# Kernel optimization log

Measured on AMD Instinct MI355X. Metric: run time of the kernel, lower is better.

Reference implementation:

```python
import jax, jax.numpy as jnp
import numpy as np

B, DIM, H, W = 8, 64, 64, 64
N_EMBED = 512
NNZ = 4          # num_nonzero OMP iterations
REG = 1e-7       # tiny Tikhonov term for the batched normal-equation solves


def batch_omp(X, D, S):
    """Batch OMP: for each signal pick S atoms greedily and solve LS on support.
    X: [N, d] signals, D: [d, K] dictionary with unit-norm atoms.
    Returns dense sparse code [N, K] with <= S nonzeros per row.
    Mathematically equivalent to the incremental-Cholesky Batch_OMP: at each
    step we solve G_II gamma = alpha0_I on the current support I.
    """
    N, K = X.shape[0], D.shape[1]
    G = D.T @ D                 # [K, K] Gram matrix (precomputed once)
    alpha0 = X @ D              # [N, K] initial correlations D^T x
    alpha = alpha0
    idx_cols = []
    gamma = None
    idx = None
    for k in range(S):          # static small loop over sparsity level
        j = jnp.argmax(jnp.abs(alpha), axis=1)                # [N] greedy atom
        idx_cols.append(j)
        idx = jnp.stack(idx_cols, axis=1)                     # [N, k+1]
        G_sub = G[idx[:, :, None], idx[:, None, :]]           # [N, k+1, k+1]
        rhs = jnp.take_along_axis(alpha0, idx, axis=1)        # [N, k+1]
        reg = REG * jnp.eye(k + 1, dtype=G.dtype)
        gamma = jnp.linalg.solve(G_sub + reg, rhs[..., None])[..., 0]  # [N, k+1]
        # residual correlations: alpha = alpha0 - G[:, I] gamma  (G symmetric)
        alpha = alpha0 - jnp.einsum('nak,na->nk', G[idx], gamma)
    code = jnp.zeros((N, K), X.dtype).at[jnp.arange(N)[:, None], idx].set(gamma)
    return code


def setup_inputs() -> dict:
    key = jax.random.key(0)
    kx, kd = jax.random.split(key)
    x = jax.random.normal(kx, (B, DIM, H, W), dtype=jnp.float32)
    dictionary = jax.random.normal(kd, (DIM, N_EMBED), dtype=jnp.float32)
    return {"x": x, "dictionary": dictionary}


def reference(x, dictionary):
    perm = jnp.transpose(x, (0, 2, 3, 1))            # [B, H, W, C]
    flat = perm.reshape(-1, DIM)                     # [N, C], N = B*H*W
    # normalize_dict=True: atoms normalized to unit L2 norm (in-place in torch)
    Dn = dictionary / jnp.linalg.norm(dictionary, axis=0, keepdims=True)
    code = batch_omp(flat, Dn, NNZ)                  # [N, K] (torch keeps [K, N])
    quant = (code @ Dn.T).reshape(perm.shape)        # reconstruction
    diff_enc = jnp.mean((quant - perm) ** 2)
    diff_dict = diff_enc                             # backward_dict=False branch
    # straight-through: perm + (quant - perm).detach() == quant in value
    out = jnp.transpose(quant, (0, 3, 1, 2))         # [B, C, H, W]
    ids = jnp.transpose(code.reshape(B, H, W, N_EMBED), (0, 3, 1, 2))  # [B, K, H, W]
    norm_0 = jnp.sum(code != 0, axis=1).astype(jnp.float32)  # L0 per signal, [N]
    num_steps = jnp.float32(NNZ)
    mean_D = jnp.mean(jnp.abs(Dn))
    mean_Z = jnp.mean(jnp.abs(code))
    norm_Z = jnp.mean(norm_0)
    topk_num = max(1, int(norm_0.shape[0] * 0.01))   # static: 327
    top_percentile = jnp.min(jax.lax.top_k(norm_0, topk_num)[0])
    num_zeros = jnp.sum(norm_0 == 0).astype(jnp.float32)
    return (out, diff_enc, diff_dict, ids, num_steps, mean_D, mean_Z,
            norm_Z, top_percentile, num_zeros)
```

## Files before the change

### kernel.cpp

```cpp
#include <hip/hip_runtime.h>
#include <cstdint>
#include <cstddef>

#define BQ 8
#define CDIM 64
#define HQ 64
#define WQ 64
#define KDIM 512
#define N_SIG 32768
#define S_NNZ 4

#define DIFF_ENC_OFF 2097152
#define DIFF_DICT_OFF 2097153
#define IDS_OFF 2097154
#define NUM_STEPS_OFF 18874370
#define MEAN_D_OFF 18874371
#define MEAN_Z_OFF 18874372
#define NORM_Z_OFF 18874373
#define TOP_PCT_OFF 18874374
#define NUM_ZEROS_OFF 18874375

#define WS_PD 16
#define WS_DNT 24
#define WS_G 32792
#define WS_WG 294936
#define WS_WI 426008

typedef float v2f __attribute__((ext_vector_type(2)));

__global__ __launch_bounds__(256) void k_ga(const float* __restrict__ X,
                                            const float* __restrict__ D,
                                            float* __restrict__ A0,
                                            float* __restrict__ G,
                                            float* __restrict__ DnT,
                                            float* __restrict__ pd,
                                            float* __restrict__ W) {
  __shared__ float Xs[64 * 64];
  __shared__ float Dns[64 * 64];
  __shared__ float partA[4][64];
  __shared__ float partB[4][64];
  __shared__ float invA[64];
  __shared__ float invB[64];
  int tid = threadIdx.x;
  int w = tid & 63, cq = tid >> 6;
  int ty = tid >> 4, tx = tid & 15;
  if (blockIdx.x == 0 && tid < 16) ((unsigned int*)W)[tid] = 0u;

  if (blockIdx.x < 64) {
    int ti = (int)blockIdx.x >> 3, tj = (int)blockIdx.x & 7;
#pragma unroll
    for (int p = 0; p < 16; ++p) {
      int c = p * 4 + cq;
      Xs[c * 64 + w] = D[(size_t)c * KDIM + ti * 64 + w];
      Dns[c * 64 + w] = D[(size_t)c * KDIM + tj * 64 + w];
    }
    __syncthreads();
    float ssA = 0.f, ssB = 0.f;
#pragma unroll
    for (int cc = 0; cc < 16; ++cc) {
      int c = cq * 16 + cc;
      float a = Xs[c * 64 + w];
      ssA = fmaf(a, a, ssA);
      float bv = Dns[c * 64 + w];
      ssB = fmaf(bv, bv, ssB);
    }
    partA[cq][w] = ssA;
    partB[cq][w] = ssB;
    __syncthreads();
    if (tid < 64) {
      invA[tid] = 1.0f / sqrtf(partA[0][tid] + partA[1][tid] + partA[2][tid] + partA[3][tid]);
      invB[tid] = 1.0f / sqrtf(partB[0][tid] + partB[1][tid] + partB[2][tid] + partB[3][tid]);
    }
    __syncthreads();
    if (ti == tj) {
      int kl = tid >> 2, cp = (tid & 3) * 16;
      float ia = invA[kl];
      float sabs = 0.f;
#pragma unroll
      for (int i = 0; i < 16; ++i) {
        int c = cp + i;
        float v = Xs[c * 64 + kl] * ia;
        DnT[(size_t)(ti * 64 + kl) * CDIM + c] = v;
        sabs += fabsf(v);
      }
#pragma unroll
      for (int off = 32; off >= 1; off >>= 1) sabs += __shfl_xor(sabs, off);
      __syncthreads();
      if ((tid & 63) == 0) partA[0][tid >> 6] = sabs;
      __syncthreads();
      if (tid == 0) pd[ti] = partA[0][0] + partA[0][1] + partA[0][2] + partA[0][3];
    }
    v2f acc[4][2] = {};
    for (int c = 0; c < 64; ++c) {
      float4 avv = *(const float4*)&Xs[c * 64 + ty * 4];
      float av[4] = {avv.x, avv.y, avv.z, avv.w};
      float4 bv = *(const float4*)&Dns[c * 64 + tx * 4];
      v2f b0 = {bv.x, bv.y}, b1 = {bv.z, bv.w};
#pragma unroll
      for (int i = 0; i < 4; ++i) {
        v2f a2 = {av[i], av[i]};
        acc[i][0] = __builtin_elementwise_fma(a2, b0, acc[i][0]);
        acc[i][1] = __builtin_elementwise_fma(a2, b1, acc[i][1]);
      }
    }
    float sn[4] = {invB[tx * 4], invB[tx * 4 + 1], invB[tx * 4 + 2], invB[tx * 4 + 3]};
#pragma unroll
    for (int i = 0; i < 4; ++i) {
      float im = invA[ty * 4 + i];
      float4 st = make_float4(acc[i][0].x * im * sn[0], acc[i][0].y * im * sn[1],
                              acc[i][1].x * im * sn[2], acc[i][1].y * im * sn[3]);
      *(float4*)&G[(size_t)(ti * 64 + ty * 4 + i) * KDIM + tj * 64 + tx * 4] = st;
    }
  } else {
    int bb = (int)blockIdx.x - 64;
    int mt = bb >> 3, nt = bb & 7;
    int b = mt >> 6, h = mt & 63;
#pragma unroll
    for (int p = 0; p < 16; ++p) {
      int c = p * 4 + cq;
      Xs[c * 64 + w] = X[(((size_t)b * CDIM + c) * HQ + h) * WQ + w];
      Dns[c * 64 + w] = D[(size_t)c * KDIM + nt * 64 + w];
    }
    __syncthreads();
    float ssB = 0.f;
#pragma unroll
    for (int cc = 0; cc < 16; ++cc) {
      int c = cq * 16 + cc;
      float bv = Dns[c * 64 + w];
      ssB = fmaf(bv, bv, ssB);
    }
    partB[cq][w] = ssB;
    __syncthreads();
    if (tid < 64)
      invB[tid] = 1.0f / sqrtf(partB[0][tid] + partB[1][tid] + partB[2][tid] + partB[3][tid]);
    __syncthreads();
    v2f acc[4][2] = {};
    for (int c = 0; c < 64; ++c) {
      float4 avv = *(const float4*)&Xs[c * 64 + ty * 4];
      float av[4] = {avv.x, avv.y, avv.z, avv.w};
      float4 bv = *(const float4*)&Dns[c * 64 + tx * 4];
      v2f b0 = {bv.x, bv.y}, b1 = {bv.z, bv.w};
#pragma unroll
      for (int i = 0; i < 4; ++i) {
        v2f a2 = {av[i], av[i]};
        acc[i][0] = __builtin_elementwise_fma(a2, b0, acc[i][0]);
        acc[i][1] = __builtin_elementwise_fma(a2, b1, acc[i][1]);
      }
    }
    float sn[4] = {invB[tx * 4], invB[tx * 4 + 1], invB[tx * 4 + 2], invB[tx * 4 + 3]};
    size_t n0 = (size_t)mt * 64;
#pragma unroll
    for (int i = 0; i < 4; ++i) {
      float4 st = make_float4(acc[i][0].x * sn[0], acc[i][0].y * sn[1],
                              acc[i][1].x * sn[2], acc[i][1].y * sn[3]);
      *(float4*)&A0[(n0 + ty * 4 + i) * KDIM + nt * 64 + tx * 4] = st;
    }
  }
}

__device__ __forceinline__ float wave_absmax_u(float m) {
#define DPP_MAX(ctrl)                                                              \
  {                                                                                \
    int t_ = __builtin_amdgcn_update_dpp(0, __float_as_int(m), (ctrl), 0xf, 0xf,   \
                                         true);                                    \
    m = fmaxf(m, __int_as_float(t_));                                              \
  }
  DPP_MAX(0x111) DPP_MAX(0x112) DPP_MAX(0x114) DPP_MAX(0x118)
  DPP_MAX(0x142) DPP_MAX(0x143)
#undef DPP_MAX
  return __int_as_float(__builtin_amdgcn_readlane(__float_as_int(m), 63));
}

template <int SZ>
__device__ __forceinline__ void solve_sz(const float (&gs)[4][4], const float (&rhs)[4],
                                         float (&gamma)[4]) {
  float M[SZ][SZ];
  float y[SZ];
  float idg[SZ];
#pragma unroll
  for (int a = 0; a < SZ; ++a) {
    y[a] = rhs[a];
#pragma unroll
    for (int b = 0; b < SZ; ++b) M[a][b] = gs[a][b] + (a == b ? 1e-7f : 0.0f);
  }
#pragma unroll
  for (int p = 0; p < SZ; ++p) {
    float ip = __builtin_amdgcn_rcpf(M[p][p]);
    idg[p] = ip;
#pragma unroll
    for (int r = p + 1; r < SZ; ++r) {
      float f = M[r][p] * ip;
#pragma unroll
      for (int c = p + 1; c < SZ; ++c) M[r][c] = fmaf(-f, M[p][c], M[r][c]);
      y[r] = fmaf(-f, y[p], y[r]);
    }
  }
#pragma unroll
  for (int r = SZ - 1; r >= 0; --r) {
    float t = y[r];
#pragma unroll
    for (int c = r + 1; c < SZ; ++c) t = fmaf(-M[r][c], gamma[c], t);
    gamma[r] = t * idg[r];
  }
}

template <int K>
__device__ __forceinline__ void omp_step(int lane, int n, const float* __restrict__ G,
                                         const float* __restrict__ A0,
                                         float (&a0)[8], float (&al)[8], float (&Grow)[3][8],
                                         float (&gs)[4][4], float (&rhs)[4], int (&idx)[4],
                                         float (&gamma)[4]) {
  float mx0 = fabsf(al[0]);
#pragma unroll
  for (int m = 1; m < 8; ++m) mx0 = fmaxf(mx0, fabsf(al[m]));
  float mx = wave_absmax_u(mx0);
  int sk = 1 << 30;
#pragma unroll
  for (int m = 0; m < 8; ++m) {
    unsigned long long bm = __ballot(fabsf(al[m]) == mx);
    if (bm) {
      int kk = (int)__builtin_ctzll(bm) * 8 + m;
      sk = kk < sk ? kk : sk;
    }
  }
  idx[K] = sk;

  const float* grow_base = G + (size_t)sk * KDIM;
  if constexpr (K < 3) {
    const float4* gp = (const float4*)(grow_base + lane * 8);
    float4 r0 = gp[0], r1 = gp[1];
    Grow[K][0] = r0.x; Grow[K][1] = r0.y; Grow[K][2] = r0.z; Grow[K][3] = r0.w;
    Grow[K][4] = r1.x; Grow[K][5] = r1.y; Grow[K][6] = r1.z; Grow[K][7] = r1.w;
  }

#pragma unroll
  for (int b = 0; b < K; ++b) {
    float v = grow_base[idx[b]];
    gs[K][b] = v;
    gs[b][K] = v;
  }
  gs[K][K] = grow_base[sk];
  rhs[K] = A0[(size_t)n * KDIM + sk];

  solve_sz<K + 1>(gs, rhs, gamma);

  if constexpr (K < 3) {
#pragma unroll
    for (int m = 0; m < 8; ++m) {
      float acc = a0[m];
#pragma unroll
      for (int a = 0; a <= K; ++a) acc = fmaf(-gamma[a], Grow[a][m], acc);
      al[m] = acc;
    }
  }
}

__global__ __launch_bounds__(256) void k_omp(const float* __restrict__ A0,
                                             const float* __restrict__ G,
                                             float4* __restrict__ wg, int4* __restrict__ wi) {
  int tid = threadIdx.x;
  int lane = tid & 63;
  int wv = __builtin_amdgcn_readfirstlane(tid >> 6);
  int n = blockIdx.x * 4 + wv;
  const float4* ap = (const float4*)(A0 + (size_t)n * KDIM + lane * 8);
  float4 v0 = ap[0], v1 = ap[1];
  float a0[8] = {v0.x, v0.y, v0.z, v0.w, v1.x, v1.y, v1.z, v1.w};
  float al[8];
#pragma unroll
  for (int m = 0; m < 8; ++m) al[m] = a0[m];
  float Grow[3][8];
  float gs[4][4];
  float rhs[4];
  int idx[4];
  float gamma[4];
  omp_step<0>(lane, n, G, A0, a0, al, Grow, gs, rhs, idx, gamma);
  omp_step<1>(lane, n, G, A0, a0, al, Grow, gs, rhs, idx, gamma);
  omp_step<2>(lane, n, G, A0, a0, al, Grow, gs, rhs, idx, gamma);
  omp_step<3>(lane, n, G, A0, a0, al, Grow, gs, rhs, idx, gamma);
  bool k0 = (idx[0] != idx[1]) && (idx[0] != idx[2]) && (idx[0] != idx[3]);
  bool k1 = (idx[1] != idx[2]) && (idx[1] != idx[3]);
  bool k2 = (idx[2] != idx[3]);
  if (lane == 0) {
    wg[n] = make_float4(k0 ? gamma[0] : 0.f, k1 ? gamma[1] : 0.f,
                        k2 ? gamma[2] : 0.f, gamma[3]);
    wi[n] = make_int4(idx[0], idx[1], idx[2], idx[3]);
  }
}

__global__ __launch_bounds__(256) void k_ei(const float* __restrict__ X,
                                            const float* __restrict__ DnT,
                                            const float4* __restrict__ wg,
                                            const int4* __restrict__ wi,
                                            float* __restrict__ out,
                                            double* __restrict__ accs,
                                            int* __restrict__ hist) {
  __shared__ __align__(16) int sIdx[64][4];
  __shared__ __align__(16) float sKg[64][4];
  __shared__ float q[64 * 65];
  __shared__ float red[4];
  int tid = threadIdx.x;

  if (blockIdx.x < 512) {
    int bh = blockIdx.x;
    int b = bh >> 6, h = bh & 63;
    if (tid < 64) {
      int w = tid;
      int n = bh * 64 + w;
      int4 iv = wi[n];
      float4 gv = wg[n];
      sIdx[w][0] = iv.x; sIdx[w][1] = iv.y; sIdx[w][2] = iv.z; sIdx[w][3] = iv.w;
      sKg[w][0] = gv.x; sKg[w][1] = gv.y; sKg[w][2] = gv.z; sKg[w][3] = gv.w;
      int nz = (int)(gv.x != 0.f) + (int)(gv.y != 0.f) +
               (int)(gv.z != 0.f) + (int)(gv.w != 0.f);
      float s = fabsf(gv.x) + fabsf(gv.y) + fabsf(gv.z) + fabsf(gv.w);
#pragma unroll
      for (int off = 32; off >= 1; off >>= 1) s += __shfl_xor(s, off);
#pragma unroll
      for (int v = 0; v < 5; ++v) {
        unsigned long long m = __ballot(nz == v);
        if (tid == 0) {
          int c = (int)__popcll(m);
          if (c) atomicAdd(&hist[v], c);
        }
      }
      if (tid == 0) atomicAdd(&accs[0], (double)s);
    }
    __syncthreads();

    int w2 = tid & 63, p = tid >> 6, c0 = p * 16;
    float acc[16] = {};
#pragma unroll
    for (int s = 0; s < 4; ++s) {
      int ks = sIdx[w2][s];
      float g = sKg[w2][s];
      const float4* dp = (const float4*)(DnT + (size_t)ks * CDIM + c0);
#pragma unroll
      for (int i4 = 0; i4 < 4; ++i4) {
        float4 d = dp[i4];
        acc[i4 * 4 + 0] = fmaf(g, d.x, acc[i4 * 4 + 0]);
        acc[i4 * 4 + 1] = fmaf(g, d.y, acc[i4 * 4 + 1]);
        acc[i4 * 4 + 2] = fmaf(g, d.z, acc[i4 * 4 + 2]);
        acc[i4 * 4 + 3] = fmaf(g, d.w, acc[i4 * 4 + 3]);
      }
    }
#pragma unroll
    for (int i = 0; i < 16; ++i) q[(c0 + i) * 65 + w2] = acc[i];
    __syncthreads();

    float sumsq = 0.f;
#pragma unroll
    for (int pass = 0; pass < 16; ++pass) {
      int c = pass * 4 + p;
      float qv = q[c * 65 + w2];
      size_t off = (((size_t)b * CDIM + c) * HQ + h) * WQ + w2;
      float xv = X[off];
      float d = qv - xv;
      sumsq = fmaf(d, d, sumsq);
      out[off] = qv;
    }

#pragma unroll
    for (int off = 32; off >= 1; off >>= 1) sumsq += __shfl_xor(sumsq, off);
    if ((tid & 63) == 0) red[tid >> 6] = sumsq;
    __syncthreads();
    if (tid == 0) atomicAdd(&accs[1], (double)(red[0] + red[1] + red[2] + red[3]));
  } else {
    int bid = blockIdx.x - 512;
    int bh = bid >> 2, kq = bid & 3;
    int b = bh >> 6, h = bh & 63;
    if (tid < 64) {
      int n = bh * 64 + tid;
      *(int4*)&sIdx[tid][0] = wi[n];
      *(float4*)&sKg[tid][0] = wg[n];
    }
    __syncthreads();
    int w4 = (tid & 15) * 4, kl = tid >> 4;
    int4 I0 = *(const int4*)&sIdx[w4][0];
    int4 I1 = *(const int4*)&sIdx[w4 + 1][0];
    int4 I2 = *(const int4*)&sIdx[w4 + 2][0];
    int4 I3 = *(const int4*)&sIdx[w4 + 3][0];
    float4 G0 = *(const float4*)&sKg[w4][0];
    float4 G1 = *(const float4*)&sKg[w4 + 1][0];
    float4 G2 = *(const float4*)&sKg[w4 + 2][0];
    float4 G3 = *(const float4*)&sKg[w4 + 3][0];
    float* ids = out + IDS_OFF;
    size_t base = (((size_t)b * KDIM + kq * 128 + kl) * HQ + h) * WQ + w4;
#pragma unroll
    for (int pass = 0; pass < 8; ++pass) {
      int k = kq * 128 + pass * 16 + kl;
      float4 v;
      v.x = (k == I0.w) ? G0.w : (k == I0.z) ? G0.z : (k == I0.y) ? G0.y : (k == I0.x) ? G0.x : 0.f;
      v.y = (k == I1.w) ? G1.w : (k == I1.z) ? G1.z : (k == I1.y) ? G1.y : (k == I1.x) ? G1.x : 0.f;
      v.z = (k == I2.w) ? G2.w : (k == I2.z) ? G2.z : (k == I2.y) ? G2.y : (k == I2.x) ? G2.x : 0.f;
      v.w = (k == I3.w) ? G3.w : (k == I3.z) ? G3.z : (k == I3.y) ? G3.y : (k == I3.x) ? G3.x : 0.f;
      *(float4*)&ids[base + (size_t)pass * 16 * 4096] = v;
    }
  }
}

__global__ __launch_bounds__(64) void k_final(const double* __restrict__ accs,
                                              const int* __restrict__ hist,
                                              const float* __restrict__ pd,
                                              float* __restrict__ out) {
  if (threadIdx.x == 0) {
    float sumAbsD = 0.f;
#pragma unroll
    for (int i = 0; i < 8; ++i) sumAbsD += pd[i];
    double sumAbsZ = accs[0], sumSq = accs[1];
    float diff = (float)(sumSq / 2097152.0);
    out[DIFF_ENC_OFF] = diff;
    out[DIFF_DICT_OFF] = diff;
    out[NUM_STEPS_OFF] = 4.0f;
    out[MEAN_D_OFF] = sumAbsD / 32768.0f;
    out[MEAN_Z_OFF] = (float)(sumAbsZ / 16777216.0);
    int h0 = hist[0], h1 = hist[1], h2 = hist[2], h3 = hist[3], h4 = hist[4];
    out[NORM_Z_OFF] = (float)((double)(h1 + 2 * h2 + 3 * h3 + 4 * h4) / 32768.0);
    int cum = 0, res = 0;
    for (int v = 4; v >= 0; --v) {
      cum += hist[v];
      if (cum >= 327) { res = v; break; }
    }
    out[TOP_PCT_OFF] = (float)res;
    out[NUM_ZEROS_OFF] = (float)h0;
  }
}

extern "C" void kernel_launch(void* const* d_in, const int* in_sizes, int n_in,
                              void* d_out, int out_size, void* d_ws, size_t ws_size,
                              hipStream_t stream) {
  (void)in_sizes; (void)n_in; (void)out_size; (void)ws_size;
  const float* X = (const float*)d_in[0];
  const float* D = (const float*)d_in[1];
  float* out = (float*)d_out;
  float* W = (float*)d_ws;
  double* accs = (double*)d_ws;
  int* hist = (int*)W + 4;
  float* pd = W + WS_PD;
  float* DnT = W + WS_DNT;
  float* G = W + WS_G;
  float4* wgam = (float4*)(W + WS_WG);
  int4* widx = (int4*)(W + WS_WI);
  float* A0 = out;

  hipLaunchKernelGGL(k_ga, dim3(4160), dim3(256), 0, stream, X, D, A0, G, DnT, pd, W);
  hipLaunchKernelGGL(k_omp, dim3(8192), dim3(256), 0, stream, A0, G, wgam, widx);
  hipLaunchKernelGGL(k_ei, dim3(2560), dim3(256), 0, stream, X, DnT, wgam, widx, out, accs, hist);
  hipLaunchKernelGGL(k_final, dim3(1), dim3(64), 0, stream, accs, hist, pd, out);
}
```

Before: 172.0 us.

## Fuse correlation GEMM into OMP kernel, drop A0 round trip through global memory

```diff
diff --git a/kernel.cpp b/kernel.cpp
--- a/kernel.cpp
+++ b/kernel.cpp
@@ -26,15 +26,16 @@
 #define WS_WG 294936
 #define WS_WI 426008
 
+#define DIL_OFF 4194304
+
 typedef float v2f __attribute__((ext_vector_type(2)));
 
-__global__ __launch_bounds__(256) void k_ga(const float* __restrict__ X,
-                                            const float* __restrict__ D,
-                                            float* __restrict__ A0,
-                                            float* __restrict__ G,
-                                            float* __restrict__ DnT,
-                                            float* __restrict__ pd,
-                                            float* __restrict__ W) {
+__global__ __launch_bounds__(256) void k_g(const float* __restrict__ D,
+                                           float* __restrict__ G,
+                                           float* __restrict__ DnT,
+                                           float* __restrict__ pd,
+                                           float* __restrict__ Dil,
+                                           float* __restrict__ W) {
   __shared__ float Xs[64 * 64];
   __shared__ float Dns[64 * 64];
   __shared__ float partA[4][64];
@@ -46,115 +47,72 @@
   int ty = tid >> 4, tx = tid & 15;
   if (blockIdx.x == 0 && tid < 16) ((unsigned int*)W)[tid] = 0u;
 
-  if (blockIdx.x < 64) {
-    int ti = (int)blockIdx.x >> 3, tj = (int)blockIdx.x & 7;
-#pragma unroll
-    for (int p = 0; p < 16; ++p) {
-      int c = p * 4 + cq;
-      Xs[c * 64 + w] = D[(size_t)c * KDIM + ti * 64 + w];
-      Dns[c * 64 + w] = D[(size_t)c * KDIM + tj * 64 + w];
-    }
-    __syncthreads();
-    float ssA = 0.f, ssB = 0.f;
-#pragma unroll
-    for (int cc = 0; cc < 16; ++cc) {
-      int c = cq * 16 + cc;
-      float a = Xs[c * 64 + w];
-      ssA = fmaf(a, a, ssA);
-      float bv = Dns[c * 64 + w];
-      ssB = fmaf(bv, bv, ssB);
-    }
-    partA[cq][w] = ssA;
-    partB[cq][w] = ssB;
-    __syncthreads();
-    if (tid < 64) {
-      invA[tid] = 1.0f / sqrtf(partA[0][tid] + partA[1][tid] + partA[2][tid] + partA[3][tid]);
-      invB[tid] = 1.0f / sqrtf(partB[0][tid] + partB[1][tid] + partB[2][tid] + partB[3][tid]);
-    }
-    __syncthreads();
-    if (ti == tj) {
-      int kl = tid >> 2, cp = (tid & 3) * 16;
-      float ia = invA[kl];
-      float sabs = 0.f;
-#pragma unroll
-      for (int i = 0; i < 16; ++i) {
-        int c = cp + i;
-        float v = Xs[c * 64 + kl] * ia;
-        DnT[(size_t)(ti * 64 + kl) * CDIM + c] = v;
-        sabs += fabsf(v);
-      }
-#pragma unroll
-      for (int off = 32; off >= 1; off >>= 1) sabs += __shfl_xor(sabs, off);
-      __syncthreads();
-      if ((tid & 63) == 0) partA[0][tid >> 6] = sabs;
-      __syncthreads();
-      if (tid == 0) pd[ti] = partA[0][0] + partA[0][1] + partA[0][2] + partA[0][3];
-    }
-    v2f acc[4][2] = {};
-    for (int c = 0; c < 64; ++c) {
-      float4 avv = *(const float4*)&Xs[c * 64 + ty * 4];
-      float av[4] = {avv.x, avv.y, avv.z, avv.w};
-      float4 bv = *(const float4*)&Dns[c * 64 + tx * 4];
-      v2f b0 = {bv.x, bv.y}, b1 = {bv.z, bv.w};
-#pragma unroll
-      for (int i = 0; i < 4; ++i) {
-        v2f a2 = {av[i], av[i]};
-        acc[i][0] = __builtin_elementwise_fma(a2, b0, acc[i][0]);
-        acc[i][1] = __builtin_elementwise_fma(a2, b1, acc[i][1]);
-      }
-    }
-    float sn[4] = {invB[tx * 4], invB[tx * 4 + 1], invB[tx * 4 + 2], invB[tx * 4 + 3]};
+  int ti = (int)blockIdx.x >> 3, tj = (int)blockIdx.x & 7;
+#pragma unroll
+  for (int p = 0; p < 16; ++p) {
+    int c = p * 4 + cq;
+    Xs[c * 64 + w] = D[(size_t)c * KDIM + ti * 64 + w];
+    Dns[c * 64 + w] = D[(size_t)c * KDIM + tj * 64 + w];
+  }
+  __syncthreads();
+  float ssA = 0.f, ssB = 0.f;
+#pragma unroll
+  for (int cc = 0; cc < 16; ++cc) {
+    int c = cq * 16 + cc;
+    float a = Xs[c * 64 + w];
+    ssA = fmaf(a, a, ssA);
+    float bv = Dns[c * 64 + w];
+    ssB = fmaf(bv, bv, ssB);
+  }
+  partA[cq][w] = ssA;
+  partB[cq][w] = ssB;
+  __syncthreads();
+  if (tid < 64) {
+    invA[tid] = 1.0f / sqrtf(partA[0][tid] + partA[1][tid] + partA[2][tid] + partA[3][tid]);
+    invB[tid] = 1.0f / sqrtf(partB[0][tid] + partB[1][tid] + partB[2][tid] + partB[3][tid]);
+  }
+  __syncthreads();
+  if (ti == tj) {
+    int kl = tid >> 2, cp = (tid & 3) * 16;
+    float ia = invA[kl];
+    int kg = ti * 64 + kl;
+    int il = kg >> 3, ij = (kg >> 2) & 1, iff = kg & 3;
+    float sabs = 0.f;
+#pragma unroll
+    for (int i = 0; i < 16; ++i) {
+      int c = cp + i;
+      float v = Xs[c * 64 + kl] * ia;
+      DnT[(size_t)kg * CDIM + c] = v;
+      Dil[((c * 2 + ij) * 64 + il) * 4 + iff] = v;
+      sabs += fabsf(v);
+    }
+#pragma unroll
+    for (int off = 32; off >= 1; off >>= 1) sabs += __shfl_xor(sabs, off);
+    __syncthreads();
+    if ((tid & 63) == 0) partA[0][tid >> 6] = sabs;
+    __syncthreads();
+    if (tid == 0) pd[ti] = partA[0][0] + partA[0][1] + partA[0][2] + partA[0][3];
+  }
+  v2f acc[4][2] = {};
+  for (int c = 0; c < 64; ++c) {
+    float4 avv = *(const float4*)&Xs[c * 64 + ty * 4];
+    float av[4] = {avv.x, avv.y, avv.z, avv.w};
+    float4 bv = *(const float4*)&Dns[c * 64 + tx * 4];
+    v2f b0 = {bv.x, bv.y}, b1 = {bv.z, bv.w};
 #pragma unroll
     for (int i = 0; i < 4; ++i) {
-      float im = invA[ty * 4 + i];
-      float4 st = make_float4(acc[i][0].x * im * sn[0], acc[i][0].y * im * sn[1],
-                              acc[i][1].x * im * sn[2], acc[i][1].y * im * sn[3]);
-      *(float4*)&G[(size_t)(ti * 64 + ty * 4 + i) * KDIM + tj * 64 + tx * 4] = st;
-    }
-  } else {
-    int bb = (int)blockIdx.x - 64;
-    int mt = bb >> 3, nt = bb & 7;
-    int b = mt >> 6, h = mt & 63;
-#pragma unroll
-    for (int p = 0; p < 16; ++p) {
-      int c = p * 4 + cq;
-      Xs[c * 64 + w] = X[(((size_t)b * CDIM + c) * HQ + h) * WQ + w];
-      Dns[c * 64 + w] = D[(size_t)c * KDIM + nt * 64 + w];
-    }
-    __syncthreads();
-    float ssB = 0.f;
-#pragma unroll
-    for (int cc = 0; cc < 16; ++cc) {
-      int c = cq * 16 + cc;
-      float bv = Dns[c * 64 + w];
-      ssB = fmaf(bv, bv, ssB);
-    }
-    partB[cq][w] = ssB;
-    __syncthreads();
-    if (tid < 64)
-      invB[tid] = 1.0f / sqrtf(partB[0][tid] + partB[1][tid] + partB[2][tid] + partB[3][tid]);
-    __syncthreads();
-    v2f acc[4][2] = {};
-    for (int c = 0; c < 64; ++c) {
-      float4 avv = *(const float4*)&Xs[c * 64 + ty * 4];
-      float av[4] = {avv.x, avv.y, avv.z, avv.w};
-      float4 bv = *(const float4*)&Dns[c * 64 + tx * 4];
-      v2f b0 = {bv.x, bv.y}, b1 = {bv.z, bv.w};
-#pragma unroll
-      for (int i = 0; i < 4; ++i) {
-        v2f a2 = {av[i], av[i]};
-        acc[i][0] = __builtin_elementwise_fma(a2, b0, acc[i][0]);
-        acc[i][1] = __builtin_elementwise_fma(a2, b1, acc[i][1]);
-      }
-    }
-    float sn[4] = {invB[tx * 4], invB[tx * 4 + 1], invB[tx * 4 + 2], invB[tx * 4 + 3]};
-    size_t n0 = (size_t)mt * 64;
-#pragma unroll
-    for (int i = 0; i < 4; ++i) {
-      float4 st = make_float4(acc[i][0].x * sn[0], acc[i][0].y * sn[1],
-                              acc[i][1].x * sn[2], acc[i][1].y * sn[3]);
-      *(float4*)&A0[(n0 + ty * 4 + i) * KDIM + nt * 64 + tx * 4] = st;
-    }
+      v2f a2 = {av[i], av[i]};
+      acc[i][0] = __builtin_elementwise_fma(a2, b0, acc[i][0]);
+      acc[i][1] = __builtin_elementwise_fma(a2, b1, acc[i][1]);
+    }
+  }
+  float sn[4] = {invB[tx * 4], invB[tx * 4 + 1], invB[tx * 4 + 2], invB[tx * 4 + 3]};
+#pragma unroll
+  for (int i = 0; i < 4; ++i) {
+    float im = invA[ty * 4 + i];
+    float4 st = make_float4(acc[i][0].x * im * sn[0], acc[i][0].y * im * sn[1],
+                            acc[i][1].x * im * sn[2], acc[i][1].y * im * sn[3]);
+    *(float4*)&G[(size_t)(ti * 64 + ty * 4 + i) * KDIM + tj * 64 + tx * 4] = st;
   }
 }
 
@@ -205,24 +163,24 @@
 }
 
 template <int K>
-__device__ __forceinline__ void omp_step(int lane, int n, const float* __restrict__ G,
-                                         const float* __restrict__ A0,
-                                         float (&a0)[8], float (&al)[8], float (&Grow)[3][8],
-                                         float (&gs)[4][4], float (&rhs)[4], int (&idx)[4],
-                                         float (&gamma)[4]) {
+__device__ __forceinline__ void omp_step2(int lane, const float* __restrict__ G,
+                                          const float (&a0)[8], float (&al)[8],
+                                          float (&Grow)[3][8], float (&gs)[4][4],
+                                          float (&rhs)[4], int (&idx)[4],
+                                          float (&gamma)[4]) {
   float mx0 = fabsf(al[0]);
-#pragma unroll
-  for (int m = 1; m < 8; ++m) mx0 = fmaxf(mx0, fabsf(al[m]));
+  int mi = 0;
+#pragma unroll
+  for (int m = 1; m < 8; ++m) {
+    float v = fabsf(al[m]);
+    mi = (v > mx0) ? m : mi;
+    mx0 = fmaxf(v, mx0);
+  }
   float mx = wave_absmax_u(mx0);
-  int sk = 1 << 30;
-#pragma unroll
-  for (int m = 0; m < 8; ++m) {
-    unsigned long long bm = __ballot(fabsf(al[m]) == mx);
-    if (bm) {
-      int kk = (int)__builtin_ctzll(bm) * 8 + m;
-      sk = kk < sk ? kk : sk;
-    }
-  }
+  unsigned long long bm = __ballot(mx0 == mx);
+  int wl = (int)__builtin_ctzll(bm);
+  int mwin = __builtin_amdgcn_readlane(mi, wl);
+  int sk = wl * 8 + mwin;
   idx[K] = sk;
 
   const float* grow_base = G + (size_t)sk * KDIM;
@@ -234,56 +192,125 @@
   }
 
 #pragma unroll
-  for (int b = 0; b < K; ++b) {
-    float v = grow_base[idx[b]];
-    gs[K][b] = v;
-    gs[b][K] = v;
+  for (int b2 = 0; b2 < K; ++b2) {
+    float v = grow_base[idx[b2]];
+    gs[K][b2] = v;
+    gs[b2][K] = v;
   }
   gs[K][K] = grow_base[sk];
-  rhs[K] = A0[(size_t)n * KDIM + sk];
+  float pick = a0[0];
+#pragma unroll
+  for (int j = 1; j < 8; ++j) pick = (mwin == j) ? a0[j] : pick;
+  rhs[K] = __int_as_float(__builtin_amdgcn_readlane(__float_as_int(pick), wl));
 
   solve_sz<K + 1>(gs, rhs, gamma);
 
   if constexpr (K < 3) {
 #pragma unroll
     for (int m = 0; m < 8; ++m) {
-      float acc = a0[m];
-#pragma unroll
-      for (int a = 0; a <= K; ++a) acc = fmaf(-gamma[a], Grow[a][m], acc);
-      al[m] = acc;
-    }
-  }
-}
-
-__global__ __launch_bounds__(256) void k_omp(const float* __restrict__ A0,
-                                             const float* __restrict__ G,
-                                             float4* __restrict__ wg, int4* __restrict__ wi) {
+      float acc2 = a0[m];
+#pragma unroll
+      for (int a = 0; a <= K; ++a) acc2 = fmaf(-gamma[a], Grow[a][m], acc2);
+      al[m] = acc2;
+    }
+  }
+}
+
+__global__ __launch_bounds__(256) void k_fused(const float* __restrict__ X,
+                                               const float* __restrict__ Dil,
+                                               const float* __restrict__ G,
+                                               float4* __restrict__ wg,
+                                               int4* __restrict__ wi) {
+  __shared__ __align__(16) float DS[16 * 512];
+  __shared__ __align__(16) float Xs[64 * 16];
   int tid = threadIdx.x;
   int lane = tid & 63;
   int wv = __builtin_amdgcn_readfirstlane(tid >> 6);
-  int n = blockIdx.x * 4 + wv;
-  const float4* ap = (const float4*)(A0 + (size_t)n * KDIM + lane * 8);
-  float4 v0 = ap[0], v1 = ap[1];
-  float a0[8] = {v0.x, v0.y, v0.z, v0.w, v1.x, v1.y, v1.z, v1.w};
-  float al[8];
-#pragma unroll
-  for (int m = 0; m < 8; ++m) al[m] = a0[m];
-  float Grow[3][8];
-  float gs[4][4];
-  float rhs[4];
-  int idx[4];
-  float gamma[4];
-  omp_step<0>(lane, n, G, A0, a0, al, Grow, gs, rhs, idx, gamma);
-  omp_step<1>(lane, n, G, A0, a0, al, Grow, gs, rhs, idx, gamma);
-  omp_step<2>(lane, n, G, A0, a0, al, Grow, gs, rhs, idx, gamma);
-  omp_step<3>(lane, n, G, A0, a0, al, Grow, gs, rhs, idx, gamma);
-  bool k0 = (idx[0] != idx[1]) && (idx[0] != idx[2]) && (idx[0] != idx[3]);
-  bool k1 = (idx[1] != idx[2]) && (idx[1] != idx[3]);
-  bool k2 = (idx[2] != idx[3]);
-  if (lane == 0) {
-    wg[n] = make_float4(k0 ? gamma[0] : 0.f, k1 ? gamma[1] : 0.f,
-                        k2 ? gamma[2] : 0.f, gamma[3]);
-    wi[n] = make_int4(idx[0], idx[1], idx[2], idx[3]);
+  int bid = (int)blockIdx.x;
+  int mt = bid >> 2, w0 = (bid & 3) * 16;
+  int b = mt >> 6, h = mt & 63;
+
+#pragma unroll
+  for (int i = 0; i < 4; ++i) {
+    int flat = i * 256 + tid;
+    int c = flat >> 4, wz = flat & 15;
+    Xs[c * 16 + wz] = X[(((size_t)b * CDIM + c) * HQ + h) * WQ + w0 + wz];
+  }
+
+  v2f acc[4][4] = {};
+  const float4* Dil4 = (const float4*)Dil;
+  float4* DS4 = (float4*)DS;
+  for (int nc = 0; nc < 4; ++nc) {
+    float4 r[8];
+#pragma unroll
+    for (int i = 0; i < 8; ++i) r[i] = Dil4[nc * 2048 + i * 256 + tid];
+    __syncthreads();
+#pragma unroll
+    for (int i = 0; i < 8; ++i) DS4[i * 256 + tid] = r[i];
+    __syncthreads();
+#pragma unroll
+    for (int cc = 0; cc < 16; ++cc) {
+      float4 xv = *(const float4*)&Xs[(nc * 16 + cc) * 16 + wv * 4];
+      float4 dA = *(const float4*)&DS[(cc * 2 + 0) * 256 + lane * 4];
+      float4 dB = *(const float4*)&DS[(cc * 2 + 1) * 256 + lane * 4];
+      v2f d0 = {dA.x, dA.y}, d1 = {dA.z, dA.w}, d2 = {dB.x, dB.y}, d3 = {dB.z, dB.w};
+      v2f x0 = {xv.x, xv.x}, x1 = {xv.y, xv.y}, x2 = {xv.z, xv.z}, x3 = {xv.w, xv.w};
+      acc[0][0] = __builtin_elementwise_fma(x0, d0, acc[0][0]);
+      acc[0][1] = __builtin_elementwise_fma(x0, d1, acc[0][1]);
+      acc[0][2] = __builtin_elementwise_fma(x0, d2, acc[0][2]);
+      acc[0][3] = __builtin_elementwise_fma(x0, d3, acc[0][3]);
+      acc[1][0] = __builtin_elementwise_fma(x1, d0, acc[1][0]);
+      acc[1][1] = __builtin_elementwise_fma(x1, d1, acc[1][1]);
+      acc[1][2] = __builtin_elementwise_fma(x1, d2, acc[1][2]);
+      acc[1][3] = __builtin_elementwise_fma(x1, d3, acc[1][3]);
+      acc[2][0] = __builtin_elementwise_fma(x2, d0, acc[2][0]);
+      acc[2][1] = __builtin_elementwise_fma(x2, d1, acc[2][1]);
+      acc[2][2] = __builtin_elementwise_fma(x2, d2, acc[2][2]);
+      acc[2][3] = __builtin_elementwise_fma(x2, d3, acc[2][3]);
+      acc[3][0] = __builtin_elementwise_fma(x3, d0, acc[3][0]);
+      acc[3][1] = __builtin_elementwise_fma(x3, d1, acc[3][1]);
+      acc[3][2] = __builtin_elementwise_fma(x3, d2, acc[3][2]);
+      acc[3][3] = __builtin_elementwise_fma(x3, d3, acc[3][3]);
+    }
+  }
+
+  int nb = mt * 64 + w0 + wv * 4;
+#pragma unroll 1
+  for (int s = 0; s < 4; ++s) {
+    float a0[8];
+    if (s == 0) {
+      a0[0] = acc[0][0].x; a0[1] = acc[0][0].y; a0[2] = acc[0][1].x; a0[3] = acc[0][1].y;
+      a0[4] = acc[0][2].x; a0[5] = acc[0][2].y; a0[6] = acc[0][3].x; a0[7] = acc[0][3].y;
+    } else if (s == 1) {
+      a0[0] = acc[1][0].x; a0[1] = acc[1][0].y; a0[2] = acc[1][1].x; a0[3] = acc[1][1].y;
+      a0[4] = acc[1][2].x; a0[5] = acc[1][2].y; a0[6] = acc[1][3].x; a0[7] = acc[1][3].y;
+    } else if (s == 2) {
+      a0[0] = acc[2][0].x; a0[1] = acc[2][0].y; a0[2] = acc[2][1].x; a0[3] = acc[2][1].y;
+      a0[4] = acc[2][2].x; a0[5] = acc[2][2].y; a0[6] = acc[2][3].x; a0[7] = acc[2][3].y;
+    } else {
+      a0[0] = acc[3][0].x; a0[1] = acc[3][0].y; a0[2] = acc[3][1].x; a0[3] = acc[3][1].y;
+      a0[4] = acc[3][2].x; a0[5] = acc[3][2].y; a0[6] = acc[3][3].x; a0[7] = acc[3][3].y;
+    }
+    float al[8];
+#pragma unroll
+    for (int m = 0; m < 8; ++m) al[m] = a0[m];
+    float Grow[3][8];
+    float gs[4][4];
+    float rhs[4];
+    int idx[4];
+    float gamma[4];
+    omp_step2<0>(lane, G, a0, al, Grow, gs, rhs, idx, gamma);
+    omp_step2<1>(lane, G, a0, al, Grow, gs, rhs, idx, gamma);
+    omp_step2<2>(lane, G, a0, al, Grow, gs, rhs, idx, gamma);
+    omp_step2<3>(lane, G, a0, al, Grow, gs, rhs, idx, gamma);
+    bool k0 = (idx[0] != idx[1]) && (idx[0] != idx[2]) && (idx[0] != idx[3]);
+    bool k1 = (idx[1] != idx[2]) && (idx[1] != idx[3]);
+    bool k2 = (idx[2] != idx[3]);
+    if (lane == 0) {
+      wg[nb + s] = make_float4(k0 ? gamma[0] : 0.f, k1 ? gamma[1] : 0.f,
+                               k2 ? gamma[2] : 0.f, gamma[3]);
+      wi[nb + s] = make_int4(idx[0], idx[1], idx[2], idx[3]);
+    }
   }
 }
 
@@ -440,10 +467,10 @@
   float* G = W + WS_G;
   float4* wgam = (float4*)(W + WS_WG);
   int4* widx = (int4*)(W + WS_WI);
-  float* A0 = out;
-
-  hipLaunchKernelGGL(k_ga, dim3(4160), dim3(256), 0, stream, X, D, A0, G, DnT, pd, W);
-  hipLaunchKernelGGL(k_omp, dim3(8192), dim3(256), 0, stream, A0, G, wgam, widx);
+  float* Dil = out + DIL_OFF;
+
+  hipLaunchKernelGGL(k_g, dim3(64), dim3(256), 0, stream, D, G, DnT, pd, Dil, W);
+  hipLaunchKernelGGL(k_fused, dim3(2048), dim3(256), 0, stream, X, Dil, G, wgam, widx);
   hipLaunchKernelGGL(k_ei, dim3(2560), dim3(256), 0, stream, X, DnT, wgam, widx, out, accs, hist);
   hipLaunchKernelGGL(k_final, dim3(1), dim3(64), 0, stream, accs, hist, pd, out);
 }
```

Result: slower. 236.1 us (+37.3%).
